# Performance work log

Measured on AMD Instinct MI355X. Metric: run time of the kernel, lower is better.

## Reference

```python
import jax, jax.numpy as jnp
import numpy as np

B, X, C = 8, 256, 256  # batch, feature axis, topfreq

def setup_inputs() -> dict:
    key = jax.random.key(0)
    k1, k2, k3, k4 = jax.random.split(key, 4)
    return {
        "amplitude": jax.random.normal(k1, (B, X, C), dtype=jnp.float32),
        "phase": jax.random.normal(k2, (B, X, C), dtype=jnp.float32),
        "A": jax.random.normal(k3, (C, C), dtype=jnp.float32),
        "w_amplitude": jnp.asarray(0.5, dtype=jnp.float32),
        "w_phase": jnp.asarray(0.5, dtype=jnp.float32),
        # uniform noise for gumbel sampling; keep away from 0 to avoid -log(-log(0))
        "gumbel_u": jax.random.uniform(k4, (B, C, C, 2), dtype=jnp.float32, minval=1e-6, maxval=1.0),
    }

def reference(amplitude, phase, A, w_amplitude, w_phase, gumbel_u):
    # pairwise diffs: (b, x, c, c)
    a_diff = amplitude[..., :, None] - amplitude[..., None, :]
    p_diff = phase[..., :, None] - phase[..., None, :]
    fused = w_amplitude * a_diff + w_phase * p_diff
    # einsum 'dd,bxcd->bxcd' == multiply by diag(A) along last dim
    temp = jnp.diagonal(A) * fused
    # einsum 'bxcd,bxcd->bcd' == sum of squares over x
    dist = jnp.sum(temp * temp, axis=1)  # (b, c, c)
    exp_dist = 1.0 / (dist + 1e-10)
    eye = jnp.eye(C, dtype=exp_dist.dtype)
    off_diag = 1.0 - eye
    exp_dist = exp_dist * off_diag
    exp_max = jax.lax.stop_gradient(jnp.max(exp_dist, axis=-1, keepdims=True))
    p = exp_dist / exp_max
    p = (p * off_diag + eye) * 0.99  # (b, c, c) in (0, 0.99]
    # bernoulli via 2-class gumbel-softmax (tau=1, hard, straight-through)
    logit = jnp.log(p / (1.0 - p))
    logits = jnp.stack([logit, -logit], axis=-1)  # (b, c, c, 2)
    g = -jnp.log(-jnp.log(gumbel_u))
    y = jax.nn.softmax(logits + g, axis=-1)
    y0 = y[..., 0]
    hard0 = (y0 > y[..., 1]).astype(y.dtype)
    sample = hard0 - jax.lax.stop_gradient(y0) + y0  # straight-through
    mask = sample.mean(axis=0)  # (c, c)
    return mask
```

## Files before the change

### kernel.cpp

```cpp
#include <hip/hip_runtime.h>

#define BB 8
#define XX 256
#define CC 256
#define TC 4
#define G  8
#define NG (XX / G)


#define STEP(CA, CP, ACC) {                                          \
    float adf   = __fsub_rn(CA, av);                                 \
    float pdf   = __fsub_rn(CP, pv);                                 \
    float fused = __fadd_rn(__fmul_rn(wa, adf), __fmul_rn(wp, pdf)); \
    float temp  = __fmul_rn(dAd, fused);                             \
    ACC = __fadd_rn(ACC, __fmul_rn(temp, temp));                     \
}

#define LOADG(BA, BP, GIDX) {                                        \
    const float* _a = ampbd + (size_t)(GIDX) * G * CC;               \
    const float* _p = phbd  + (size_t)(GIDX) * G * CC;               \
    _Pragma("unroll")                                                \
    for (int i = 0; i < G; ++i) {                                    \
        BA[i] = _a[(size_t)i * CC];                                  \
        BP[i] = _p[(size_t)i * CC];                                  \
    }                                                                \
}

#define COMPG(BA, BP, GIDX) {                                        \
    const int _xb = (GIDX) * G;                                      \
    _Pragma("unroll")                                                \
    for (int i = 0; i < G; ++i) {                                    \
        const float av = BA[i];                                      \
        const float pv = BP[i];                                      \
        const float4 ca = colsA[_xb + i];                            \
        const float4 cp = colsP[_xb + i];                            \
        STEP(ca.x, cp.x, acc0)                                       \
        STEP(ca.y, cp.y, acc1)                                       \
        STEP(ca.z, cp.z, acc2)                                       \
        STEP(ca.w, cp.w, acc3)                                       \
    }                                                                \
}

__global__ __launch_bounds__(256, 2) void mahal_mask_kernel(
    const float* __restrict__ amp,
    const float* __restrict__ ph,
    const float* __restrict__ A,
    const float* __restrict__ wAp,
    const float* __restrict__ wPp,
    const float* __restrict__ gu,
    float* __restrict__ out)
{
    const int d  = threadIdx.x;
    const int c0 = blockIdx.x * TC;
    const int b  = blockIdx.y;

    const float wa = wAp[0];
    const float wp = wPp[0];

    __shared__ float4 colsA[XX];
    __shared__ float4 colsP[XX];
    {
        const int x = threadIdx.x;
        const size_t base = (size_t)b * XX * CC + (size_t)x * CC + c0;
        colsA[x] = *(const float4*)(amp + base);
        colsP[x] = *(const float4*)(ph  + base);
    }
    __syncthreads();

    const float dAd = A[(size_t)d * CC + d];

    float acc0 = 0.0f, acc1 = 0.0f, acc2 = 0.0f, acc3 = 0.0f;

    const float* ampbd = amp + (size_t)b * XX * CC + d;
    const float* phbd  = ph  + (size_t)b * XX * CC + d;

    float b0A[G], b0P[G], b1A[G], b1P[G];

    LOADG(b0A, b0P, 0)
    for (int g = 0; g + 2 < NG; g += 2) {
        LOADG(b1A, b1P, g + 1)
        COMPG(b0A, b0P, g)
        LOADG(b0A, b0P, g + 2)
        COMPG(b1A, b1P, g + 1)
    }
    LOADG(b1A, b1P, NG - 1)
    COMPG(b0A, b0P, NG - 2)
    COMPG(b1A, b1P, NG - 1)

    float ed[TC];
    ed[0] = (d == c0)     ? 0.0f : __fdiv_rn(1.0f, __fadd_rn(acc0, 1e-10f));
    ed[1] = (d == c0 + 1) ? 0.0f : __fdiv_rn(1.0f, __fadd_rn(acc1, 1e-10f));
    ed[2] = (d == c0 + 2) ? 0.0f : __fdiv_rn(1.0f, __fadd_rn(acc2, 1e-10f));
    ed[3] = (d == c0 + 3) ? 0.0f : __fdiv_rn(1.0f, __fadd_rn(acc3, 1e-10f));

    __shared__ float wmax[TC][4];
    const int wave = threadIdx.x >> 6;
    const int lane = threadIdx.x & 63;
#pragma unroll
    for (int j = 0; j < TC; ++j) {
        float v = ed[j];
#pragma unroll
        for (int m = 1; m < 64; m <<= 1) v = fmaxf(v, __shfl_xor(v, m));
        if (lane == 0) wmax[j][wave] = v;
    }
    __syncthreads();

#pragma unroll
    for (int j = 0; j < TC; ++j) {
        const int c = c0 + j;
        float em = fmaxf(fmaxf(wmax[j][0], wmax[j][1]), fmaxf(wmax[j][2], wmax[j][3]));
        float p;
        if (d == c) {
            p = 0.99f;
        } else {
            p = __fmul_rn(__fdiv_rn(ed[j], em), 0.99f);
        }
        float logit = logf(__fdiv_rn(p, __fsub_rn(1.0f, p)));

        const float2 g2 = *(const float2*)(gu + (((size_t)b * CC + c) * CC + d) * 2);
        float g0 = -logf(-logf(g2.x));
        float g1 = -logf(-logf(g2.y));

        float a0 = __fadd_rn(logit, g0);
        float a1 = __fadd_rn(-logit, g1);
        float m  = fmaxf(a0, a1);
        float e0 = expf(__fsub_rn(a0, m));
        float e1 = expf(__fsub_rn(a1, m));
        float s  = __fadd_rn(e0, e1);
        float y0 = __fdiv_rn(e0, s);
        float y1 = __fdiv_rn(e1, s);
        if (y0 > y1) {
            atomicAdd(&out[(size_t)c * CC + d], 0.125f);
        }
    }
}

extern "C" void kernel_launch(void* const* d_in, const int* in_sizes, int n_in,
                              void* d_out, int out_size, void* d_ws, size_t ws_size,
                              hipStream_t stream) {
    const float* amp = (const float*)d_in[0];
    const float* ph  = (const float*)d_in[1];
    const float* A   = (const float*)d_in[2];
    const float* wa  = (const float*)d_in[3];
    const float* wp  = (const float*)d_in[4];
    const float* gu  = (const float*)d_in[5];
    float* out = (float*)d_out;

    hipMemsetAsync(out, 0, (size_t)CC * CC * sizeof(float), stream);

    dim3 grid(CC / TC, BB);
    mahal_mask_kernel<<<grid, 256, 0, stream>>>(amp, ph, A, wa, wp, gu, out);
}
```

Measured before the change: 103.8 us.

## Precombine weighted amplitude/phase and split x reduction across two kernels

Uses linearity to compute u = wa*amp + wp*ph once per element, so each pair step is one subtraction instead of two subtractions and a blend. When workspace allows, the x-axis reduction is split into two halves over a 3D grid, which doubles the block count for occupancy. Partial distances go to workspace and a second kernel sums them and runs the Gumbel epilogue. This adds a workspace round trip and an extra launch, and changes rounding slightly because the weighted sum is now taken before the difference.

```diff
diff --git a/kernel.cpp b/kernel.cpp
--- a/kernel.cpp
+++ b/kernel.cpp
@@ -5,77 +5,48 @@
 #define CC 256
 #define TC 4
 #define G  8
-#define NG (XX / G)
-
-
-#define STEP(CA, CP, ACC) {                                          \
-    float adf   = __fsub_rn(CA, av);                                 \
-    float pdf   = __fsub_rn(CP, pv);                                 \
-    float fused = __fadd_rn(__fmul_rn(wa, adf), __fmul_rn(wp, pdf)); \
-    float temp  = __fmul_rn(dAd, fused);                             \
-    ACC = __fadd_rn(ACC, __fmul_rn(temp, temp));                     \
-}
-
-#define LOADG(BA, BP, GIDX) {                                        \
-    const float* _a = ampbd + (size_t)(GIDX) * G * CC;               \
-    const float* _p = phbd  + (size_t)(GIDX) * G * CC;               \
-    _Pragma("unroll")                                                \
-    for (int i = 0; i < G; ++i) {                                    \
-        BA[i] = _a[(size_t)i * CC];                                  \
-        BP[i] = _p[(size_t)i * CC];                                  \
-    }                                                                \
-}
-
-#define COMPG(BA, BP, GIDX) {                                        \
-    const int _xb = (GIDX) * G;                                      \
-    _Pragma("unroll")                                                \
-    for (int i = 0; i < G; ++i) {                                    \
-        const float av = BA[i];                                      \
-        const float pv = BP[i];                                      \
-        const float4 ca = colsA[_xb + i];                            \
-        const float4 cp = colsP[_xb + i];                            \
-        STEP(ca.x, cp.x, acc0)                                       \
-        STEP(ca.y, cp.y, acc1)                                       \
-        STEP(ca.z, cp.z, acc2)                                       \
-        STEP(ca.w, cp.w, acc3)                                       \
-    }                                                                \
-}
-
-__global__ __launch_bounds__(256, 2) void mahal_mask_kernel(
-    const float* __restrict__ amp,
-    const float* __restrict__ ph,
-    const float* __restrict__ A,
-    const float* __restrict__ wAp,
-    const float* __restrict__ wPp,
-    const float* __restrict__ gu,
-    float* __restrict__ out)
-{
-    const int d  = threadIdx.x;
-    const int c0 = blockIdx.x * TC;
-    const int b  = blockIdx.y;
-
-    const float wa = wAp[0];
-    const float wp = wPp[0];
-
-    __shared__ float4 colsA[XX];
-    __shared__ float4 colsP[XX];
-    {
-        const int x = threadIdx.x;
-        const size_t base = (size_t)b * XX * CC + (size_t)x * CC + c0;
-        colsA[x] = *(const float4*)(amp + base);
-        colsP[x] = *(const float4*)(ph  + base);
-    }
-    __syncthreads();
-
-    const float dAd = A[(size_t)d * CC + d];
-
-    float acc0 = 0.0f, acc1 = 0.0f, acc2 = 0.0f, acc3 = 0.0f;
-
-    const float* ampbd = amp + (size_t)b * XX * CC + d;
-    const float* phbd  = ph  + (size_t)b * XX * CC + d;
-
+
+
+#define STEPU(UC, ACC) {                         \
+    float diff = __fsub_rn(UC, ud);              \
+    float t    = __fmul_rn(dAd, diff);           \
+    float sq   = __fmul_rn(t, t);                \
+    ACC = __fadd_rn(ACC, sq);                    \
+}
+
+#define LOADG(BA, BP, GIDX) {                    \
+    const float* _a = ampbd + (size_t)(GIDX) * G * CC; \
+    const float* _p = phbd  + (size_t)(GIDX) * G * CC; \
+    _Pragma("unroll")                            \
+    for (int i = 0; i < G; ++i) {                \
+        BA[i] = _a[(size_t)i * CC];              \
+        BP[i] = _p[(size_t)i * CC];              \
+    }                                            \
+}
+
+#define COMPG(BA, BP, GIDX) {                    \
+    const int _xb = (GIDX) * G;                  \
+    _Pragma("unroll")                            \
+    for (int i = 0; i < G; ++i) {                \
+        const float av = BA[i];                  \
+        const float pv = BP[i];                  \
+        const float ud = __fadd_rn(__fmul_rn(wa, av), __fmul_rn(wp, pv)); \
+        const float4 uc = cols[_xb + i];         \
+        STEPU(uc.x, acc0)                        \
+        STEPU(uc.y, acc1)                        \
+        STEPU(uc.z, acc2)                        \
+        STEPU(uc.w, acc3)                        \
+    }                                            \
+}
+
+template<int XPB>
+__device__ __forceinline__ void dist_loop(
+    const float* __restrict__ ampbd, const float* __restrict__ phbd,
+    const float4* cols, float wa, float wp, float dAd,
+    float& acc0, float& acc1, float& acc2, float& acc3)
+{
+    constexpr int NG = XPB / G;
     float b0A[G], b0P[G], b1A[G], b1P[G];
-
     LOADG(b0A, b0P, 0)
     for (int g = 0; g + 2 < NG; g += 2) {
         LOADG(b1A, b1P, g + 1)
@@ -86,14 +57,39 @@
     LOADG(b1A, b1P, NG - 1)
     COMPG(b0A, b0P, NG - 2)
     COMPG(b1A, b1P, NG - 1)
-
+}
+
+template<int XPB>
+__device__ __forceinline__ void stage_cols(
+    const float* __restrict__ amp, const float* __restrict__ ph,
+    int b, int x0, int c0, float wa, float wp, float4* cols)
+{
+    if (threadIdx.x < XPB) {
+        const int x = threadIdx.x;
+        const size_t base = ((size_t)b * XX + (x0 + x)) * CC + c0;
+        const float4 a4 = *(const float4*)(amp + base);
+        const float4 p4 = *(const float4*)(ph  + base);
+        float4 u;
+        u.x = __fadd_rn(__fmul_rn(wa, a4.x), __fmul_rn(wp, p4.x));
+        u.y = __fadd_rn(__fmul_rn(wa, a4.y), __fmul_rn(wp, p4.y));
+        u.z = __fadd_rn(__fmul_rn(wa, a4.z), __fmul_rn(wp, p4.z));
+        u.w = __fadd_rn(__fmul_rn(wa, a4.w), __fmul_rn(wp, p4.w));
+        cols[x] = u;
+    }
+    __syncthreads();
+}
+
+__device__ __forceinline__ void epilogue(
+    float dist0, float dist1, float dist2, float dist3,
+    int b, int c0, int d, const float* __restrict__ gu,
+    float* __restrict__ out, float (*wmax)[4])
+{
     float ed[TC];
-    ed[0] = (d == c0)     ? 0.0f : __fdiv_rn(1.0f, __fadd_rn(acc0, 1e-10f));
-    ed[1] = (d == c0 + 1) ? 0.0f : __fdiv_rn(1.0f, __fadd_rn(acc1, 1e-10f));
-    ed[2] = (d == c0 + 2) ? 0.0f : __fdiv_rn(1.0f, __fadd_rn(acc2, 1e-10f));
-    ed[3] = (d == c0 + 3) ? 0.0f : __fdiv_rn(1.0f, __fadd_rn(acc3, 1e-10f));
-
-    __shared__ float wmax[TC][4];
+    ed[0] = (d == c0)     ? 0.0f : __fdiv_rn(1.0f, __fadd_rn(dist0, 1e-10f));
+    ed[1] = (d == c0 + 1) ? 0.0f : __fdiv_rn(1.0f, __fadd_rn(dist1, 1e-10f));
+    ed[2] = (d == c0 + 2) ? 0.0f : __fdiv_rn(1.0f, __fadd_rn(dist2, 1e-10f));
+    ed[3] = (d == c0 + 3) ? 0.0f : __fdiv_rn(1.0f, __fadd_rn(dist3, 1e-10f));
+
     const int wave = threadIdx.x >> 6;
     const int lane = threadIdx.x & 63;
 #pragma unroll
@@ -135,6 +131,85 @@
     }
 }
 
+
+__global__ __launch_bounds__(256, 4) void k_dist(
+    const float* __restrict__ amp, const float* __restrict__ ph,
+    const float* __restrict__ A,   const float* __restrict__ wAp,
+    const float* __restrict__ wPp, float* __restrict__ wsd)
+{
+    const int d    = threadIdx.x;
+    const int c0   = blockIdx.x * TC;
+    const int b    = blockIdx.y;
+    const int half = blockIdx.z;
+    const int x0   = half * (XX / 2);
+
+    const float wa = wAp[0];
+    const float wp = wPp[0];
+
+    __shared__ float4 cols[XX / 2];
+    stage_cols<XX / 2>(amp, ph, b, x0, c0, wa, wp, cols);
+
+    const float dAd = A[(size_t)d * CC + d];
+    const float* ampbd = amp + ((size_t)b * XX + x0) * CC + d;
+    const float* phbd  = ph  + ((size_t)b * XX + x0) * CC + d;
+
+    float acc0 = 0.0f, acc1 = 0.0f, acc2 = 0.0f, acc3 = 0.0f;
+    dist_loop<XX / 2>(ampbd, phbd, cols, wa, wp, dAd, acc0, acc1, acc2, acc3);
+
+    float* w = wsd + (((size_t)half * BB + b) * CC + c0) * CC + d;
+    w[0 * CC] = acc0;
+    w[1 * CC] = acc1;
+    w[2 * CC] = acc2;
+    w[3 * CC] = acc3;
+}
+
+__global__ __launch_bounds__(256, 2) void k_epi(
+    const float* __restrict__ wsd, const float* __restrict__ gu,
+    float* __restrict__ out)
+{
+    const int d  = threadIdx.x;
+    const int c0 = blockIdx.x * TC;
+    const int b  = blockIdx.y;
+
+    const float* w0 = wsd + (((size_t)0 * BB + b) * CC + c0) * CC + d;
+    const float* w1 = wsd + (((size_t)1 * BB + b) * CC + c0) * CC + d;
+    float dist0 = __fadd_rn(w0[0 * CC], w1[0 * CC]);
+    float dist1 = __fadd_rn(w0[1 * CC], w1[1 * CC]);
+    float dist2 = __fadd_rn(w0[2 * CC], w1[2 * CC]);
+    float dist3 = __fadd_rn(w0[3 * CC], w1[3 * CC]);
+
+    __shared__ float wmax[TC][4];
+    epilogue(dist0, dist1, dist2, dist3, b, c0, d, gu, out, wmax);
+}
+
+
+__global__ __launch_bounds__(256, 2) void k_fused(
+    const float* __restrict__ amp, const float* __restrict__ ph,
+    const float* __restrict__ A,   const float* __restrict__ wAp,
+    const float* __restrict__ wPp, const float* __restrict__ gu,
+    float* __restrict__ out)
+{
+    const int d  = threadIdx.x;
+    const int c0 = blockIdx.x * TC;
+    const int b  = blockIdx.y;
+
+    const float wa = wAp[0];
+    const float wp = wPp[0];
+
+    __shared__ float4 cols[XX];
+    stage_cols<XX>(amp, ph, b, 0, c0, wa, wp, cols);
+
+    const float dAd = A[(size_t)d * CC + d];
+    const float* ampbd = amp + (size_t)b * XX * CC + d;
+    const float* phbd  = ph  + (size_t)b * XX * CC + d;
+
+    float acc0 = 0.0f, acc1 = 0.0f, acc2 = 0.0f, acc3 = 0.0f;
+    dist_loop<XX>(ampbd, phbd, cols, wa, wp, dAd, acc0, acc1, acc2, acc3);
+
+    __shared__ float wmax[TC][4];
+    epilogue(acc0, acc1, acc2, acc3, b, c0, d, gu, out, wmax);
+}
+
 extern "C" void kernel_launch(void* const* d_in, const int* in_sizes, int n_in,
                               void* d_out, int out_size, void* d_ws, size_t ws_size,
                               hipStream_t stream) {
@@ -148,6 +223,15 @@
 
     hipMemsetAsync(out, 0, (size_t)CC * CC * sizeof(float), stream);
 
-    dim3 grid(CC / TC, BB);
-    mahal_mask_kernel<<<grid, 256, 0, stream>>>(amp, ph, A, wa, wp, gu, out);
-}
+    const size_t need = 2ull * BB * CC * CC * sizeof(float);
+    if (ws_size >= need) {
+        float* wsd = (float*)d_ws;
+        dim3 g1(CC / TC, BB, 2);
+        k_dist<<<g1, 256, 0, stream>>>(amp, ph, A, wa, wp, wsd);
+        dim3 g2(CC / TC, BB);
+        k_epi<<<g2, 256, 0, stream>>>(wsd, gu, out);
+    } else {
+        dim3 g(CC / TC, BB);
+        k_fused<<<g, 256, 0, stream>>>(amp, ph, A, wa, wp, gu, out);
+    }
+}
```

New measurement: 92.00 us. -11.3%, faster.
